# Performance work log

Hardware: AMD Instinct MI355X
Metric: run time of the kernel (lower is better)

The kernel has to match this reference:

```python
import jax, jax.numpy as jnp
import numpy as np

D_MODEL = 1024
N_HEADS = 16
D_HEAD = D_MODEL // N_HEADS
WIN = 128        # local_window
HALF = WIN // 2  # 64
KW = 2 * WIN     # kv window length per block (half-left + block + half-right)


def setup_inputs() -> dict:
    key = jax.random.key(0)
    ks = jax.random.split(key, 6)
    B, L = 2, 8192
    s = 0.02
    return {
        "x": jax.random.normal(ks[0], (B, L, D_MODEL), dtype=jnp.float32),
        "wq": jax.random.normal(ks[1], (D_MODEL, D_MODEL), dtype=jnp.float32) * s,
        "wk": jax.random.normal(ks[2], (D_MODEL, D_MODEL), dtype=jnp.float32) * s,
        "wv": jax.random.normal(ks[3], (D_MODEL, D_MODEL), dtype=jnp.float32) * s,
        "wo": jax.random.normal(ks[4], (D_MODEL, D_MODEL), dtype=jnp.float32) * s,
        "bo": jax.random.normal(ks[5], (D_MODEL,), dtype=jnp.float32) * s,
    }


def _rotate_half(t):
    t1, t2 = jnp.split(t, 2, axis=-1)
    return jnp.concatenate([-t2, t1], axis=-1)


def _rope(L, dtype):
    inv_freq = 1.0 / (10000.0 ** (jnp.arange(0, D_HEAD, 2, dtype=jnp.float32) / D_HEAD))
    t = jnp.arange(L, dtype=jnp.float32)
    freqs = t[:, None] * inv_freq[None, :]          # [L, D_HEAD/2]
    emb = jnp.concatenate([freqs, freqs], axis=-1)  # [L, D_HEAD]
    return jnp.cos(emb).astype(dtype), jnp.sin(emb).astype(dtype)


def reference(x, wq, wk, wv, wo, bo):
    B, L, D = x.shape
    H, Dh = N_HEADS, D_HEAD
    # projections (torch Linear: x @ W.T)
    q = (x @ wq.T).reshape(B, L, H, Dh).transpose(0, 2, 1, 3)  # [B,H,L,Dh]
    k = (x @ wk.T).reshape(B, L, H, Dh).transpose(0, 2, 1, 3)
    v = (x @ wv.T).reshape(B, L, H, Dh).transpose(0, 2, 1, 3)
    cos, sin = _rope(L, x.dtype)                    # [L, Dh]
    q = q * cos + _rotate_half(q) * sin
    k = k * cos + _rotate_half(k) * sin
    nb = L // WIN
    starts = jnp.arange(nb) * WIN - HALF            # window start per block
    idx = starts[:, None] + jnp.arange(KW)          # [nb, KW] kv indices
    valid = (idx >= 0) & (idx < L)
    idxc = jnp.clip(idx, 0, L - 1)
    kw = k[:, :, idxc]                              # [B,H,nb,KW,Dh]
    vw = v[:, :, idxc]
    qb = q.reshape(B, H, nb, WIN, Dh)
    scores = jnp.einsum('bhnqd,bhnkd->bhnqk', qb, kw) / np.sqrt(Dh).astype(x.dtype)
    scores = jnp.where(valid[None, None, :, None, :], scores, -jnp.inf)
    attn = jax.nn.softmax(scores, axis=-1)
    out = jnp.einsum('bhnqk,bhnkd->bhnqd', attn, vw).reshape(B, H, L, Dh)
    out = out.transpose(0, 2, 1, 3).reshape(B, L, D)
    return out @ wo.T + bo
```

## Files before the change

kernel.cpp:

```cpp
#include <hip/hip_runtime.h>
#include <cstdint>
#include <math.h>

#define L_SEQ 8192
#define DM    1024
#define NQK   2048

typedef unsigned short u16;
typedef __bf16 bf16;
typedef bf16  bf16x8 __attribute__((ext_vector_type(8)));
typedef float f32x4  __attribute__((ext_vector_type(4)));

__device__ __forceinline__ u16 f2bf(float f) {
    unsigned u = __float_as_uint(f);
    u += 0x7fffu + ((u >> 16) & 1u);
    return (u16)(u >> 16);
}

__device__ __forceinline__ f32x4 mfma16(bf16x8 a, bf16x8 b, f32x4 c) {
    return __builtin_amdgcn_mfma_f32_16x16x32_bf16(a, b, c, 0, 0, 0);
}

__device__ __forceinline__ void gld_lds16(const u16* g, u16* l) {
    __builtin_amdgcn_global_load_lds((const __attribute__((address_space(1))) void*)g,
                                     (__attribute__((address_space(3))) void*)l,
                                     16, 0, 0);
}

__device__ __forceinline__ void bar() {
    __builtin_amdgcn_s_barrier();
}
#define LGKMCNT0() asm volatile("s_waitcnt lgkmcnt(0)" ::: "memory")
#define VMCNT8()  asm volatile("s_waitcnt vmcnt(8)" ::: "memory")
#define VMCNT0()  asm volatile("s_waitcnt vmcnt(0)" ::: "memory")

__global__ void cvt_bf16(const float* __restrict__ src, u16* __restrict__ dst, int n8) {
    int i = blockIdx.x * 256 + threadIdx.x;
    if (i >= n8) return;
    const float4* s4 = (const float4*)src;
    float4 a = s4[2 * i], b = s4[2 * i + 1];
    union { uint4 u; u16 h[8]; } r;
    r.h[0] = f2bf(a.x); r.h[1] = f2bf(a.y); r.h[2] = f2bf(a.z); r.h[3] = f2bf(a.w);
    r.h[4] = f2bf(b.x); r.h[5] = f2bf(b.y); r.h[6] = f2bf(b.z); r.h[7] = f2bf(b.w);
    ((uint4*)dst)[i] = r.u;
}

__global__ void rope_tbl(float2* __restrict__ t) {
    int idx = blockIdx.x * 256 + threadIdx.x;
    int pos = idx >> 5, i = idx & 31;
    float invf = exp2f(-0.4152410118609191f * (float)i);
    float s, c;
    sincosf((float)pos * invf, &s, &c);
    t[idx] = make_float2(c, s);
}


#define STAGE_A(kt, ha, par) do { \
    gld_lds16(baseA + (size_t)(ha) * 131072 + (size_t)(kt) * 64, \
              ldsA + (par) * 16384 + (ha) * 8192); \
    gld_lds16(baseA + (size_t)(ha) * 131072 + 65536 + (size_t)(kt) * 64, \
              ldsA + (par) * 16384 + (ha) * 8192 + 4096); \
} while (0)
#define STAGE_B(kt, hb, par) do { \
    gld_lds16(baseB + (size_t)(hb) * 131072 + (size_t)(kt) * 64, \
              ldsB + (par) * 16384 + (hb) * 8192); \
    gld_lds16(baseB + (size_t)(hb) * 131072 + 65536 + (size_t)(kt) * 64, \
              ldsB + (par) * 16384 + (hb) * 8192 + 4096); \
} while (0)

#define K_LOOP_PIPELINED()                                                     \
                       \
    STAGE_A(0, 0, 0); STAGE_A(0, 1, 0);                                        \
    STAGE_B(0, 0, 0); STAGE_B(0, 1, 0);                                        \
    STAGE_A(1, 0, 1); STAGE_A(1, 1, 1);                                        \
    STAGE_B(1, 0, 1); STAGE_B(1, 1, 1);                                        \
    VMCNT8();                                                                  \
    bar();                                                                     \
    bf16x8 pA[8], pB[4], qA[8], qB[4];                                         \
    {                                                                          \
        const u16* pa0 = SA + aoff;                                            \
        const u16* pb0 = SB + boff;                                            \
        _Pragma("unroll")                                                      \
        for (int m = 0; m < 8; m++) pA[m] = *(const bf16x8*)(pa0 + m * 1024 + c0); \
        _Pragma("unroll")                                                      \
        for (int n = 0; n < 4; n++) pB[n] = *(const bf16x8*)(pb0 + n * 1024 + c0); \
    }                                                                          \
    _Pragma("unroll 2")                                                        \
    for (int u = 0; u < 16; ++u) {                                             \
        const int par = u & 1;                                                 \
        const u16* pa = SA + par * 16384 + aoff;                               \
        const u16* pb = SB + par * 16384 + boff;                               \
        const u16* qa = SA + (par ^ 1) * 16384 + aoff;                         \
        const u16* qb = SB + (par ^ 1) * 16384 + boff;                         \
                                \
        _Pragma("unroll")                                                      \
        for (int m = 0; m < 8; m++) qA[m] = *(const bf16x8*)(pa + m * 1024 + c1); \
        _Pragma("unroll")                                                      \
        for (int n = 0; n < 4; n++) qB[n] = *(const bf16x8*)(pb + n * 1024 + c1); \
        __builtin_amdgcn_s_setprio(1);                                         \
        _Pragma("unroll")                                                      \
        for (int m = 0; m < 8; m++)                                            \
            _Pragma("unroll")                                                  \
            for (int n = 0; n < 4; n++)                                        \
                acc[m][n] = mfma16(pA[m], pB[n], acc[m][n]);                   \
        __builtin_amdgcn_s_setprio(0);                                         \
        LGKMCNT0();         \
        VMCNT0();            \
        bar();                                                                 \
        __builtin_amdgcn_sched_barrier(0);                                     \
         \
        _Pragma("unroll")                                                      \
        for (int m = 0; m < 8; m++) pA[m] = *(const bf16x8*)(qa + m * 1024 + c0); \
        _Pragma("unroll")                                                      \
        for (int n = 0; n < 4; n++) pB[n] = *(const bf16x8*)(qb + n * 1024 + c0); \
        STAGE_A((u + 2) & 15, 0, par); STAGE_A((u + 2) & 15, 1, par);          \
        STAGE_B((u + 2) & 15, 0, par); STAGE_B((u + 2) & 15, 1, par);          \
        __builtin_amdgcn_s_setprio(1);                                         \
        _Pragma("unroll")                                                      \
        for (int m = 0; m < 8; m++)                                            \
            _Pragma("unroll")                                                  \
            for (int n = 0; n < 4; n++)                                        \
                acc[m][n] = mfma16(qA[m], qB[n], acc[m][n]);                   \
        __builtin_amdgcn_s_setprio(0);                                         \
    }                                                                          \
    VMCNT0();                                                                  \
    LGKMCNT0();                                                                \
    bar();

__global__ __launch_bounds__(512, 2) void gemm_qkv_fused(
    const u16* __restrict__ X,
    const u16* __restrict__ W,
    const float2* __restrict__ rope,
    u16* __restrict__ Y,
    u16* __restrict__ Vt)
{
    __shared__ __align__(16) u16 smem[65536];
    u16* SA = smem;
    u16* SB = smem + 32768;

    const int o   = (int)blockIdx.x;
    const int xcd = o & 7;
    const int r   = o >> 3;
    const int st  = r >> 5;
    const int t   = r & 31;
    const int m0  = (xcd * 8 + (t & 7)) * 256;
    const int n0  = (st * 4 + (t >> 3)) * 256;

    const int tid = threadIdx.x;
    const int lane = tid & 63, w = tid >> 6;
    const int wm = w >> 2, wn = w & 3;
    const int quad = lane >> 4, ln = lane & 15;

    const int r0 = tid >> 3;
    const int cgs = (tid & 7) ^ (r0 & 7);
    const u16* baseA = X + (size_t)(m0 + r0) * DM + cgs * 8;
    const u16* baseB = W + (size_t)(n0 + r0) * DM + cgs * 8;
    u16* ldsA = SA + tid * 8;
    u16* ldsB = SB + tid * 8;

    const int c0 = (quad ^ (ln & 7)) * 8;
    const int c1 = ((quad + 4) ^ (ln & 7)) * 8;
    const int aoff = wm * 8192 + ln * 64;
    const int boff = (wn >> 1) * 8192 + ((wn & 1) * 64 + ln) * 64;

    const f32x4 fz = {0.f, 0.f, 0.f, 0.f};
    f32x4 acc[8][4];
    #pragma unroll
    for (int a = 0; a < 8; a++)
        #pragma unroll
        for (int b = 0; b < 4; b++) acc[a][b] = fz;

    K_LOOP_PIPELINED();

    if (n0 < 2048) {
        #pragma unroll
        for (int mt = 0; mt < 8; mt++)
            #pragma unroll
            for (int reg = 0; reg < 4; reg++) {
                int rg = (m0 + wm * 128 + mt * 16 + quad * 4 + reg) & (L_SEQ - 1);
                const float2* rp = rope + rg * 32;
                #pragma unroll
                for (int nt = 0; nt < 2; nt++) {
                    float2 cs = rp[nt * 16 + ln];
                    float x1 = acc[mt][nt][reg], x2 = acc[mt][nt + 2][reg];
                    acc[mt][nt][reg]     = x1 * cs.x - x2 * cs.y;
                    acc[mt][nt + 2][reg] = x2 * cs.x + x1 * cs.y;
                }
            }
        u16* Es = smem;
        #pragma unroll
        for (int mh = 0; mh < 2; mh++) {
            if (mh) __syncthreads();
            if (wm == mh) {
                #pragma unroll
                for (int mt = 0; mt < 8; mt++)
                    #pragma unroll
                    for (int nt = 0; nt < 4; nt++)
                        #pragma unroll
                        for (int reg = 0; reg < 4; reg++)
                            Es[(mt * 16 + quad * 4 + reg) * 264 + wn * 64 + nt * 16 + ln] =
                                f2bf(acc[mt][nt][reg]);
            }
            __syncthreads();
            #pragma unroll
            for (int i = 0; i < 8; i++) {
                int idx = i * 512 + tid;
                int row = idx >> 5, ch = (idx & 31) * 8;
                uint4 v = *(const uint4*)(Es + row * 264 + ch);
                *(uint4*)(Y + (size_t)(m0 + mh * 128 + row) * NQK + n0 + ch) = v;
            }
        }
    } else {
        u16* Es = smem;
        const int bb = m0 >> 13, seq0 = m0 & (L_SEQ - 1);
        #pragma unroll
        for (int nh = 0; nh < 2; nh++) {
            if (nh) __syncthreads();
            if ((wn >> 1) == nh) {
                #pragma unroll
                for (int mt = 0; mt < 8; mt++)
                    #pragma unroll
                    for (int nt = 0; nt < 4; nt++)
                        #pragma unroll
                        for (int reg = 0; reg < 4; reg++)
                            Es[((wn & 1) * 64 + nt * 16 + ln) * 264 + wm * 128 + mt * 16 + quad * 4 + reg] =
                                f2bf(acc[mt][nt][reg]);
            }
            __syncthreads();
            #pragma unroll
            for (int i = 0; i < 8; i++) {
                int idx = i * 512 + tid;
                int dr = idx >> 5, ch = (idx & 31) * 8;
                int gc = n0 - 2048 + nh * 128 + dr;
                uint4 v = *(const uint4*)(Es + dr * 264 + ch);
                *(uint4*)(Vt + (size_t)(bb * 1024 + gc) * L_SEQ + seq0 + ch) = v;
            }
        }
    }
}

__global__ __launch_bounds__(512, 2) void gemm_oproj(
    const u16* __restrict__ A,
    const u16* __restrict__ Wo,
    const float* __restrict__ bias,
    float* __restrict__ Out)
{
    __shared__ __align__(16) u16 smem[65536];
    u16* SA = smem;
    u16* SB = smem + 32768;

    const int o   = (int)blockIdx.x;
    const int xcd = o & 7;
    const int t   = o >> 3;
    const int m0  = (xcd * 8 + (t & 7)) * 256;
    const int n0  = (t >> 3) * 256;

    const int tid = threadIdx.x;
    const int lane = tid & 63, w = tid >> 6;
    const int wm = w >> 2, wn = w & 3;
    const int quad = lane >> 4, ln = lane & 15;

    const int r0 = tid >> 3;
    const int cgs = (tid & 7) ^ (r0 & 7);
    const u16* baseA = A  + (size_t)(m0 + r0) * DM + cgs * 8;
    const u16* baseB = Wo + (size_t)(n0 + r0) * DM + cgs * 8;
    u16* ldsA = SA + tid * 8;
    u16* ldsB = SB + tid * 8;

    const int c0 = (quad ^ (ln & 7)) * 8;
    const int c1 = ((quad + 4) ^ (ln & 7)) * 8;
    const int aoff = wm * 8192 + ln * 64;
    const int boff = (wn >> 1) * 8192 + ((wn & 1) * 64 + ln) * 64;

    const f32x4 fz = {0.f, 0.f, 0.f, 0.f};
    f32x4 acc[8][4];
    #pragma unroll
    for (int a = 0; a < 8; a++)
        #pragma unroll
        for (int b = 0; b < 4; b++) acc[a][b] = fz;

    K_LOOP_PIPELINED();

    float b4[4];
    #pragma unroll
    for (int nt = 0; nt < 4; nt++) b4[nt] = bias[n0 + wn * 64 + nt * 16 + ln];

    float* Ef = (float*)smem;
    #pragma unroll
    for (int mq = 0; mq < 4; mq++) {
        if (mq) __syncthreads();
        if (wm == (mq >> 1)) {
            #pragma unroll
            for (int mt = 0; mt < 4; mt++)
                #pragma unroll
                for (int nt = 0; nt < 4; nt++)
                    #pragma unroll
                    for (int reg = 0; reg < 4; reg++)
                        Ef[(mt * 16 + quad * 4 + reg) * 260 + wn * 64 + nt * 16 + ln] =
                            acc[(mq & 1) * 4 + mt][nt][reg] + b4[nt];
        }
        __syncthreads();
        #pragma unroll
        for (int i = 0; i < 8; i++) {
            int idx = i * 512 + tid;
            int row = idx >> 6, ch = (idx & 63) * 4;
            float4 v = *(const float4*)(Ef + row * 260 + ch);
            *(float4*)(Out + (size_t)(m0 + mq * 64 + row) * DM + n0 + ch) = v;
        }
    }
}

__global__ __launch_bounds__(512, 4) void attn(
    const u16* __restrict__ QK,
    const u16* __restrict__ Vt,
    u16* __restrict__ AO)
{
    __shared__ __align__(16) u16 Ks[256 * 64];
    __shared__ __align__(16) u16 Vs[64 * 256];
    __shared__ __align__(16) u16 pbuf[8][512];

    const int blk = blockIdx.x;
    const int h   = blockIdx.y;
    const int b   = blockIdx.z;
    const int tid = threadIdx.x;
    const int lane = tid & 63, w = tid >> 6;
    const int quad = lane >> 4, ln = lane & 15;
    const int wstart = blk * 128 - 64;
    const size_t bbase = (size_t)b * L_SEQ;

    const u16* Kg = QK + 1024 + h * 64;
    const u16* Vg = Vt + (size_t)(b * 1024 + h * 64) * L_SEQ;

    #pragma unroll
    for (int i = 0; i < 4; i++) {
        int c = i * 512 + tid;
        int row = c >> 3, cl = c & 7, cg = cl ^ (row & 7);
        int kr = wstart + row;
        kr = kr < 0 ? 0 : (kr > L_SEQ - 1 ? L_SEQ - 1 : kr);
        gld_lds16(Kg + (size_t)(bbase + kr) * NQK + cg * 8, Ks + c * 8);
    }
    #pragma unroll
    for (int i = 0; i < 4; i++) {
        int c = i * 512 + tid;
        int d = c >> 5, kc = c & 31, cg = kc ^ (d & 7);
        int key = wstart + cg * 8;
        key = key < 0 ? 0 : (key > L_SEQ - 8 ? L_SEQ - 8 : key);
        gld_lds16(Vg + (size_t)d * L_SEQ + key, Vs + c * 8);
    }

    const int qrow = blk * 128 + w * 16 + ln;
    const u16* qp = QK + (bbase + qrow) * NQK + h * 64 + quad * 8;
    bf16x8 aq0 = *(const bf16x8*)qp;
    bf16x8 aq1 = *(const bf16x8*)(qp + 32);
    __syncthreads();

    const f32x4 fz = {0.f, 0.f, 0.f, 0.f};
    f32x4 s[16];
    #pragma unroll
    for (int nt = 0; nt < 16; nt++) {
        int row = nt * 16 + ln;
        bf16x8 b0 = *(const bf16x8*)(Ks + row * 64 + ((quad       ^ (ln & 7)) * 8));
        bf16x8 b1 = *(const bf16x8*)(Ks + row * 64 + (((4 + quad) ^ (ln & 7)) * 8));
        f32x4 t = mfma16(aq0, b0, fz);
        t = mfma16(aq1, b1, t);
        s[nt] = t;
    }
    __syncthreads();

    const float SC = 0.125f * 1.4426950408889634f;
    float mr[4] = {-INFINITY, -INFINITY, -INFINITY, -INFINITY};
    #pragma unroll
    for (int nt = 0; nt < 16; nt++) {
        int key = wstart + nt * 16 + ln;
        bool valid = (key >= 0) && (key < L_SEQ);
        #pragma unroll
        for (int r = 0; r < 4; r++) {
            float v = valid ? s[nt][r] * SC : -INFINITY;
            s[nt][r] = v;
            mr[r] = fmaxf(mr[r], v);
        }
    }
    #pragma unroll
    for (int off = 1; off < 16; off <<= 1)
        #pragma unroll
        for (int r = 0; r < 4; r++) mr[r] = fmaxf(mr[r], __shfl_xor(mr[r], off));

    float lr[4] = {0.f, 0.f, 0.f, 0.f};
    #pragma unroll
    for (int nt = 0; nt < 16; nt++)
        #pragma unroll
        for (int r = 0; r < 4; r++) {
            float p = exp2f(s[nt][r] - mr[r]);
            s[nt][r] = p;
            lr[r] += p;
        }
    #pragma unroll
    for (int off = 1; off < 16; off <<= 1)
        #pragma unroll
        for (int r = 0; r < 4; r++) lr[r] += __shfl_xor(lr[r], off);
    float rl[4];
    #pragma unroll
    for (int r = 0; r < 4; r++) rl[r] = 1.f / lr[r];

    u16* pb = pbuf[w];
    f32x4 o[4] = {fz, fz, fz, fz};
    #pragma unroll
    for (int ks = 0; ks < 8; ks++) {
        #pragma unroll
        for (int n2 = 0; n2 < 2; n2++) {
            int nt = ks * 2 + n2;
            #pragma unroll
            for (int r = 0; r < 4; r++)
                pb[(quad * 4 + r) * 32 + ((n2 * 16 + ln) ^ (quad * 8))] = f2bf(s[nt][r]);
        }
        bf16x8 ap = *(const bf16x8*)(pb + ln * 32 + ((quad * 8) ^ (((ln >> 2) & 3) * 8)));
        #pragma unroll
        for (int dt = 0; dt < 4; dt++) {
            int d = dt * 16 + ln;
            bf16x8 vb = *(const bf16x8*)(Vs + d * 256 + (((ks * 4 + quad) ^ (ln & 7)) * 8));
            o[dt] = mfma16(ap, vb, o[dt]);
        }
    }

    u16* AOs = Ks;
    #pragma unroll
    for (int dt = 0; dt < 4; dt++)
        #pragma unroll
        for (int r = 0; r < 4; r++)
            AOs[(w * 16 + quad * 4 + r) * 72 + dt * 16 + ln] = f2bf(o[dt][r] * rl[r]);
    __syncthreads();
    #pragma unroll
    for (int i = 0; i < 2; i++) {
        int c = i * 512 + tid;
        int row = c >> 3, ch = (c & 7) * 8;
        uint4 v = *(const uint4*)(AOs + row * 72 + ch);
        *(uint4*)(AO + (bbase + blk * 128 + row) * DM + h * 64 + ch) = v;
    }
}

extern "C" void kernel_launch(void* const* d_in, const int* in_sizes, int n_in,
                              void* d_out, int out_size, void* d_ws, size_t ws_size,
                              hipStream_t stream) {
    const float* x  = (const float*)d_in[0];
    const float* wq = (const float*)d_in[1];
    const float* wk = (const float*)d_in[2];
    const float* wv = (const float*)d_in[3];
    const float* wo = (const float*)d_in[4];
    const float* bo = (const float*)d_in[5];
    float* out = (float*)d_out;

    char* ws = (char*)d_ws;
    const size_t MB = 1024 * 1024;
    u16*   xb  = (u16*)ws;
    u16*   fqk = (u16*)(ws + 32 * MB);
    u16*   vt  = (u16*)(ws + 96 * MB);
    u16*   wf  = (u16*)(ws + 128 * MB);
    float2* rt = (float2*)(ws + 134 * MB);
    u16*   wob = (u16*)(ws + 136 * MB);
    u16*   aob = xb;

    cvt_bf16<<<8192, 256, 0, stream>>>(x, xb, 2097152);
    cvt_bf16<<<512, 256, 0, stream>>>(wq, wf, 131072);
    cvt_bf16<<<512, 256, 0, stream>>>(wk, wf + 1024 * 1024, 131072);
    cvt_bf16<<<512, 256, 0, stream>>>(wv, wf + 2 * 1024 * 1024, 131072);
    cvt_bf16<<<512, 256, 0, stream>>>(wo, wob, 131072);
    rope_tbl<<<1024, 256, 0, stream>>>(rt);

    gemm_qkv_fused<<<768, 512, 0, stream>>>(xb, wf, rt, fqk, vt);
    attn<<<dim3(64, 16, 2), 512, 0, stream>>>(fqk, vt, aob);
    gemm_oproj<<<256, 512, 0, stream>>>(aob, wob, bo, out);
}
```

Before: 356.7 us.

## Restructure GEMMs to 256x128 tiles with triple-buffered fully unrolled K loop

```diff
diff --git a/kernel.cpp b/kernel.cpp
--- a/kernel.cpp
+++ b/kernel.cpp
@@ -26,13 +26,6 @@
                                      (__attribute__((address_space(3))) void*)l,
                                      16, 0, 0);
 }
-
-__device__ __forceinline__ void bar() {
-    __builtin_amdgcn_s_barrier();
-}
-#define LGKMCNT0() asm volatile("s_waitcnt lgkmcnt(0)" ::: "memory")
-#define VMCNT8()  asm volatile("s_waitcnt vmcnt(8)" ::: "memory")
-#define VMCNT0()  asm volatile("s_waitcnt vmcnt(0)" ::: "memory")
 
 __global__ void cvt_bf16(const float* __restrict__ src, u16* __restrict__ dst, int n8) {
     int i = blockIdx.x * 256 + threadIdx.x;
@@ -55,122 +48,124 @@
 }
 
 
-#define STAGE_A(kt, ha, par) do { \
-    gld_lds16(baseA + (size_t)(ha) * 131072 + (size_t)(kt) * 64, \
-              ldsA + (par) * 16384 + (ha) * 8192); \
-    gld_lds16(baseA + (size_t)(ha) * 131072 + 65536 + (size_t)(kt) * 64, \
-              ldsA + (par) * 16384 + (ha) * 8192 + 4096); \
+#define QITER(U, WIMM, RD, ST) do {                                            \
+    __builtin_amdgcn_s_waitcnt(WIMM);                                          \
+    __builtin_amdgcn_sched_barrier(0);                                         \
+    __builtin_amdgcn_s_barrier();                                              \
+    __builtin_amdgcn_sched_barrier(0);                                         \
+    if (RD) {                                                                  \
+        _Pragma("unroll")                                                      \
+        for (int m = 0; m < 8; m++)                                            \
+            fA[(U + 1) & 1][m] = *(const bf16x8*)(SAs + ((U + 1) % 3) * 8192 + aBase + m * 512); \
+        _Pragma("unroll")                                                      \
+        for (int n = 0; n < 4; n++)                                            \
+            fB[(U + 1) & 1][n] = *(const bf16x8*)(SBs + ((U + 1) % 3) * 4096 + bBase + n * 512); \
+    }                                                                          \
+    if (ST) {                                                                  \
+        _Pragma("unroll")                                                      \
+        for (int i = 0; i < 4; ++i)                                            \
+            gld_lds16(gA[i] + (U + 3) * 32, ldsAt + (U % 3) * 8192 + i * 2048);\
+        _Pragma("unroll")                                                      \
+        for (int i = 0; i < 2; ++i)                                            \
+            gld_lds16(gB[i] + (U + 3) * 32, ldsBt + (U % 3) * 4096 + i * 2048);\
+    }                                                                          \
+    __builtin_amdgcn_sched_barrier(0);                                         \
+    __builtin_amdgcn_s_setprio(1);                                             \
+    _Pragma("unroll")                                                          \
+    for (int m = 0; m < 8; m++)                                                \
+        _Pragma("unroll")                                                      \
+        for (int n = 0; n < 4; n++)                                            \
+            acc[m][n] = mfma16(fA[(U) & 1][m], fB[(U) & 1][n], acc[m][n]);     \
+    __builtin_amdgcn_s_setprio(0);                                             \
+    __builtin_amdgcn_sched_barrier(0);                                         \
 } while (0)
-#define STAGE_B(kt, hb, par) do { \
-    gld_lds16(baseB + (size_t)(hb) * 131072 + (size_t)(kt) * 64, \
-              ldsB + (par) * 16384 + (hb) * 8192); \
-    gld_lds16(baseB + (size_t)(hb) * 131072 + 65536 + (size_t)(kt) * 64, \
-              ldsB + (par) * 16384 + (hb) * 8192 + 4096); \
-} while (0)
-
-#define K_LOOP_PIPELINED()                                                     \
-                       \
-    STAGE_A(0, 0, 0); STAGE_A(0, 1, 0);                                        \
-    STAGE_B(0, 0, 0); STAGE_B(0, 1, 0);                                        \
-    STAGE_A(1, 0, 1); STAGE_A(1, 1, 1);                                        \
-    STAGE_B(1, 0, 1); STAGE_B(1, 1, 1);                                        \
-    VMCNT8();                                                                  \
-    bar();                                                                     \
-    bf16x8 pA[8], pB[4], qA[8], qB[4];                                         \
-    {                                                                          \
-        const u16* pa0 = SA + aoff;                                            \
-        const u16* pb0 = SB + boff;                                            \
-        _Pragma("unroll")                                                      \
-        for (int m = 0; m < 8; m++) pA[m] = *(const bf16x8*)(pa0 + m * 1024 + c0); \
-        _Pragma("unroll")                                                      \
-        for (int n = 0; n < 4; n++) pB[n] = *(const bf16x8*)(pb0 + n * 1024 + c0); \
+
+#define K_LOOP_ALL()                                                           \
+    QITER(0,0x0076,1,1);  QITER(1,0x0076,1,1);  QITER(2,0x0076,1,1);           \
+    QITER(3,0x0076,1,1);  QITER(4,0x0076,1,1);  QITER(5,0x0076,1,1);           \
+    QITER(6,0x0076,1,1);  QITER(7,0x0076,1,1);  QITER(8,0x0076,1,1);           \
+    QITER(9,0x0076,1,1);  QITER(10,0x0076,1,1); QITER(11,0x0076,1,1);          \
+    QITER(12,0x0076,1,1); QITER(13,0x0076,1,1); QITER(14,0x0076,1,1);          \
+    QITER(15,0x0076,1,1); QITER(16,0x0076,1,1); QITER(17,0x0076,1,1);          \
+    QITER(18,0x0076,1,1); QITER(19,0x0076,1,1); QITER(20,0x0076,1,1);          \
+    QITER(21,0x0076,1,1); QITER(22,0x0076,1,1); QITER(23,0x0076,1,1);          \
+    QITER(24,0x0076,1,1); QITER(25,0x0076,1,1); QITER(26,0x0076,1,1);          \
+    QITER(27,0x0076,1,1); QITER(28,0x0076,1,1); QITER(29,0x0076,1,0);          \
+    QITER(30,0x0070,1,0); QITER(31,0x0070,0,0)
+
+#define GEMM_SETUP()                                                           \
+    u16* SAs = smem;                                \
+    u16* SBs = smem + 24576;                        \
+    const int tid = threadIdx.x;                                               \
+    const int lane = tid & 63, w = tid >> 6;                                   \
+    const int wm = w >> 1, wn = w & 1;                                         \
+    const int quad = lane >> 4, ln = lane & 15;                                \
+    const u16* gA[4]; const u16* gB[2];                                        \
+    _Pragma("unroll")                                                          \
+    for (int i = 0; i < 4; ++i) {                                              \
+        int s = i * 256 + tid;                                                 \
+        int li = s >> 3, pc = s & 7, lc = pc ^ (li & 7);                       \
+        int row = 2 * li + (lc >> 2), kc = lc & 3;                             \
+        gA[i] = Ap + (size_t)(m0 + row) * DM + kc * 8;                         \
     }                                                                          \
-    _Pragma("unroll 2")                                                        \
-    for (int u = 0; u < 16; ++u) {                                             \
-        const int par = u & 1;                                                 \
-        const u16* pa = SA + par * 16384 + aoff;                               \
-        const u16* pb = SB + par * 16384 + boff;                               \
-        const u16* qa = SA + (par ^ 1) * 16384 + aoff;                         \
-        const u16* qb = SB + (par ^ 1) * 16384 + boff;                         \
-                                \
-        _Pragma("unroll")                                                      \
-        for (int m = 0; m < 8; m++) qA[m] = *(const bf16x8*)(pa + m * 1024 + c1); \
-        _Pragma("unroll")                                                      \
-        for (int n = 0; n < 4; n++) qB[n] = *(const bf16x8*)(pb + n * 1024 + c1); \
-        __builtin_amdgcn_s_setprio(1);                                         \
-        _Pragma("unroll")                                                      \
-        for (int m = 0; m < 8; m++)                                            \
-            _Pragma("unroll")                                                  \
-            for (int n = 0; n < 4; n++)                                        \
-                acc[m][n] = mfma16(pA[m], pB[n], acc[m][n]);                   \
-        __builtin_amdgcn_s_setprio(0);                                         \
-        LGKMCNT0();         \
-        VMCNT0();            \
-        bar();                                                                 \
-        __builtin_amdgcn_sched_barrier(0);                                     \
-         \
-        _Pragma("unroll")                                                      \
-        for (int m = 0; m < 8; m++) pA[m] = *(const bf16x8*)(qa + m * 1024 + c0); \
-        _Pragma("unroll")                                                      \
-        for (int n = 0; n < 4; n++) pB[n] = *(const bf16x8*)(qb + n * 1024 + c0); \
-        STAGE_A((u + 2) & 15, 0, par); STAGE_A((u + 2) & 15, 1, par);          \
-        STAGE_B((u + 2) & 15, 0, par); STAGE_B((u + 2) & 15, 1, par);          \
-        __builtin_amdgcn_s_setprio(1);                                         \
-        _Pragma("unroll")                                                      \
-        for (int m = 0; m < 8; m++)                                            \
-            _Pragma("unroll")                                                  \
-            for (int n = 0; n < 4; n++)                                        \
-                acc[m][n] = mfma16(qA[m], qB[n], acc[m][n]);                   \
-        __builtin_amdgcn_s_setprio(0);                                         \
+    _Pragma("unroll")                                                          \
+    for (int i = 0; i < 2; ++i) {                                              \
+        int s = i * 256 + tid;                                                 \
+        int li = s >> 3, pc = s & 7, lc = pc ^ (li & 7);                       \
+        int row = 2 * li + (lc >> 2), kc = lc & 3;                             \
+        gB[i] = Bp + (size_t)(n0 + row) * DM + kc * 8;                         \
     }                                                                          \
-    VMCNT0();                                                                  \
-    LGKMCNT0();                                                                \
-    bar();
-
-__global__ __launch_bounds__(512, 2) void gemm_qkv_fused(
+    u16* ldsAt = SAs + tid * 8;                                                \
+    u16* ldsBt = SBs + tid * 8;                                                \
+    const int l7  = (ln >> 1) & 7;                                             \
+    const int pcq = ((ln & 1) * 4 + quad) ^ l7;                                \
+    const int aBase = (wm * 64 + (ln >> 1)) * 64 + pcq * 8;                    \
+    const int bBase = (wn * 32 + (ln >> 1)) * 64 + pcq * 8;                    \
+    const f32x4 fz = {0.f, 0.f, 0.f, 0.f};                                     \
+    f32x4 acc[8][4];                                                           \
+    _Pragma("unroll")                                                          \
+    for (int a = 0; a < 8; a++)                                                \
+        _Pragma("unroll")                                                      \
+        for (int b = 0; b < 4; b++) acc[a][b] = fz;                            \
+    bf16x8 fA[2][8], fB[2][4];                                                 \
+                              \
+    _Pragma("unroll")                                                          \
+    for (int t3 = 0; t3 < 3; ++t3) {                                           \
+        _Pragma("unroll")                                                      \
+        for (int i = 0; i < 4; ++i) gld_lds16(gA[i] + t3 * 32, ldsAt + t3 * 8192 + i * 2048); \
+        _Pragma("unroll")                                                      \
+        for (int i = 0; i < 2; ++i) gld_lds16(gB[i] + t3 * 32, ldsBt + t3 * 4096 + i * 2048); \
+    }                                                                          \
+    __builtin_amdgcn_s_waitcnt(0x0F7C);        \
+    __builtin_amdgcn_s_barrier();                                              \
+    __builtin_amdgcn_sched_barrier(0);                                         \
+    _Pragma("unroll")                                                          \
+    for (int m = 0; m < 8; m++) fA[0][m] = *(const bf16x8*)(SAs + aBase + m * 512); \
+    _Pragma("unroll")                                                          \
+    for (int n = 0; n < 4; n++) fB[0][n] = *(const bf16x8*)(SBs + bBase + n * 512)
+
+__global__ __launch_bounds__(256, 2) void gemm_qkv_fused(
     const u16* __restrict__ X,
     const u16* __restrict__ W,
     const float2* __restrict__ rope,
     u16* __restrict__ Y,
     u16* __restrict__ Vt)
 {
-    __shared__ __align__(16) u16 smem[65536];
-    u16* SA = smem;
-    u16* SB = smem + 32768;
+    __shared__ __align__(16) u16 smem[36864];
 
     const int o   = (int)blockIdx.x;
     const int xcd = o & 7;
     const int r   = o >> 3;
-    const int st  = r >> 5;
-    const int t   = r & 31;
+    const int st  = r >> 6;
+    const int t   = r & 63;
     const int m0  = (xcd * 8 + (t & 7)) * 256;
-    const int n0  = (st * 4 + (t >> 3)) * 256;
-
-    const int tid = threadIdx.x;
-    const int lane = tid & 63, w = tid >> 6;
-    const int wm = w >> 2, wn = w & 3;
-    const int quad = lane >> 4, ln = lane & 15;
-
-    const int r0 = tid >> 3;
-    const int cgs = (tid & 7) ^ (r0 & 7);
-    const u16* baseA = X + (size_t)(m0 + r0) * DM + cgs * 8;
-    const u16* baseB = W + (size_t)(n0 + r0) * DM + cgs * 8;
-    u16* ldsA = SA + tid * 8;
-    u16* ldsB = SB + tid * 8;
-
-    const int c0 = (quad ^ (ln & 7)) * 8;
-    const int c1 = ((quad + 4) ^ (ln & 7)) * 8;
-    const int aoff = wm * 8192 + ln * 64;
-    const int boff = (wn >> 1) * 8192 + ((wn & 1) * 64 + ln) * 64;
-
-    const f32x4 fz = {0.f, 0.f, 0.f, 0.f};
-    f32x4 acc[8][4];
-    #pragma unroll
-    for (int a = 0; a < 8; a++)
-        #pragma unroll
-        for (int b = 0; b < 4; b++) acc[a][b] = fz;
-
-    K_LOOP_PIPELINED();
+    const int n0  = (st * 8 + (t >> 3)) * 128;
+
+    const u16* Ap = X;
+    const u16* Bp = W;
+    GEMM_SETUP();
+    K_LOOP_ALL();
+    __syncthreads();
 
     if (n0 < 2048) {
         #pragma unroll
@@ -198,15 +193,15 @@
                     for (int nt = 0; nt < 4; nt++)
                         #pragma unroll
                         for (int reg = 0; reg < 4; reg++)
-                            Es[(mt * 16 + quad * 4 + reg) * 264 + wn * 64 + nt * 16 + ln] =
+                            Es[(mt * 16 + quad * 4 + reg) * 136 + wn * 64 + nt * 16 + ln] =
                                 f2bf(acc[mt][nt][reg]);
             }
             __syncthreads();
             #pragma unroll
             for (int i = 0; i < 8; i++) {
-                int idx = i * 512 + tid;
-                int row = idx >> 5, ch = (idx & 31) * 8;
-                uint4 v = *(const uint4*)(Es + row * 264 + ch);
+                int idx = i * 256 + tid;
+                int row = idx >> 4, ch = (idx & 15) * 8;
+                uint4 v = *(const uint4*)(Es + row * 136 + ch);
                 *(uint4*)(Y + (size_t)(m0 + mh * 128 + row) * NQK + n0 + ch) = v;
             }
         }
@@ -214,72 +209,50 @@
         u16* Es = smem;
         const int bb = m0 >> 13, seq0 = m0 & (L_SEQ - 1);
         #pragma unroll
-        for (int nh = 0; nh < 2; nh++) {
-            if (nh) __syncthreads();
-            if ((wn >> 1) == nh) {
+        for (int rh = 0; rh < 2; rh++) {
+            if (rh) __syncthreads();
+            if (wm == rh) {
                 #pragma unroll
                 for (int mt = 0; mt < 8; mt++)
                     #pragma unroll
                     for (int nt = 0; nt < 4; nt++)
                         #pragma unroll
                         for (int reg = 0; reg < 4; reg++)
-                            Es[((wn & 1) * 64 + nt * 16 + ln) * 264 + wm * 128 + mt * 16 + quad * 4 + reg] =
+                            Es[(wn * 64 + nt * 16 + ln) * 136 + mt * 16 + quad * 4 + reg] =
                                 f2bf(acc[mt][nt][reg]);
             }
             __syncthreads();
             #pragma unroll
             for (int i = 0; i < 8; i++) {
-                int idx = i * 512 + tid;
-                int dr = idx >> 5, ch = (idx & 31) * 8;
-                int gc = n0 - 2048 + nh * 128 + dr;
-                uint4 v = *(const uint4*)(Es + dr * 264 + ch);
-                *(uint4*)(Vt + (size_t)(bb * 1024 + gc) * L_SEQ + seq0 + ch) = v;
+                int idx = i * 256 + tid;
+                int dr = idx >> 4, ch = (idx & 15) * 8;
+                int gc = n0 - 2048 + dr;
+                uint4 v = *(const uint4*)(Es + dr * 136 + ch);
+                *(uint4*)(Vt + (size_t)(bb * 1024 + gc) * L_SEQ + seq0 + rh * 128 + ch) = v;
             }
         }
     }
 }
 
-__global__ __launch_bounds__(512, 2) void gemm_oproj(
+__global__ __launch_bounds__(256, 2) void gemm_oproj(
     const u16* __restrict__ A,
     const u16* __restrict__ Wo,
     const float* __restrict__ bias,
     float* __restrict__ Out)
 {
-    __shared__ __align__(16) u16 smem[65536];
-    u16* SA = smem;
-    u16* SB = smem + 32768;
+    __shared__ __align__(16) u16 smem[36864];
 
     const int o   = (int)blockIdx.x;
     const int xcd = o & 7;
     const int t   = o >> 3;
     const int m0  = (xcd * 8 + (t & 7)) * 256;
-    const int n0  = (t >> 3) * 256;
-
-    const int tid = threadIdx.x;
-    const int lane = tid & 63, w = tid >> 6;
-    const int wm = w >> 2, wn = w & 3;
-    const int quad = lane >> 4, ln = lane & 15;
-
-    const int r0 = tid >> 3;
-    const int cgs = (tid & 7) ^ (r0 & 7);
-    const u16* baseA = A  + (size_t)(m0 + r0) * DM + cgs * 8;
-    const u16* baseB = Wo + (size_t)(n0 + r0) * DM + cgs * 8;
-    u16* ldsA = SA + tid * 8;
-    u16* ldsB = SB + tid * 8;
-
-    const int c0 = (quad ^ (ln & 7)) * 8;
-    const int c1 = ((quad + 4) ^ (ln & 7)) * 8;
-    const int aoff = wm * 8192 + ln * 64;
-    const int boff = (wn >> 1) * 8192 + ((wn & 1) * 64 + ln) * 64;
-
-    const f32x4 fz = {0.f, 0.f, 0.f, 0.f};
-    f32x4 acc[8][4];
-    #pragma unroll
-    for (int a = 0; a < 8; a++)
-        #pragma unroll
-        for (int b = 0; b < 4; b++) acc[a][b] = fz;
-
-    K_LOOP_PIPELINED();
+    const int n0  = (t >> 3) * 128;
+
+    const u16* Ap = A;
+    const u16* Bp = Wo;
+    GEMM_SETUP();
+    K_LOOP_ALL();
+    __syncthreads();
 
     float b4[4];
     #pragma unroll
@@ -296,15 +269,15 @@
                 for (int nt = 0; nt < 4; nt++)
                     #pragma unroll
                     for (int reg = 0; reg < 4; reg++)
-                        Ef[(mt * 16 + quad * 4 + reg) * 260 + wn * 64 + nt * 16 + ln] =
+                        Ef[(mt * 16 + quad * 4 + reg) * 132 + wn * 64 + nt * 16 + ln] =
                             acc[(mq & 1) * 4 + mt][nt][reg] + b4[nt];
         }
         __syncthreads();
         #pragma unroll
         for (int i = 0; i < 8; i++) {
-            int idx = i * 512 + tid;
-            int row = idx >> 6, ch = (idx & 63) * 4;
-            float4 v = *(const float4*)(Ef + row * 260 + ch);
+            int idx = i * 256 + tid;
+            int row = idx >> 5, ch = (idx & 31) * 4;
+            float4 v = *(const float4*)(Ef + row * 132 + ch);
             *(float4*)(Out + (size_t)(m0 + mq * 64 + row) * DM + n0 + ch) = v;
         }
     }
@@ -466,7 +439,7 @@
     cvt_bf16<<<512, 256, 0, stream>>>(wo, wob, 131072);
     rope_tbl<<<1024, 256, 0, stream>>>(rt);
 
-    gemm_qkv_fused<<<768, 512, 0, stream>>>(xb, wf, rt, fqk, vt);
+    gemm_qkv_fused<<<1536, 256, 0, stream>>>(xb, wf, rt, fqk, vt);
     attn<<<dim3(64, 16, 2), 512, 0, stream>>>(fqk, vt, aob);
-    gemm_oproj<<<256, 512, 0, stream>>>(aob, wob, bo, out);
-}
+    gemm_oproj<<<512, 256, 0, stream>>>(aob, wob, bo, out);
+}
```

New measurement: 365.7 us. 1.03x slower.
